# Optimization experiments

Measured on AMD Instinct MI355X. Metric: run time of the kernel, lower is better.

The kernel has to match this reference:

```python
import jax, jax.numpy as jnp
import numpy as np

N_NODES = 50000
N_EDGES = 800000
D = 101
L = 2
NEG_SLOPE = 0.2


def setup_inputs() -> dict:
    key = jax.random.key(0)
    k1, k2, k3, k4, k5 = jax.random.split(key, 5)
    x = jax.random.normal(k1, (N_NODES, D), dtype=jnp.float32)
    edge_index = jax.random.randint(k2, (2, N_EDGES), 0, N_NODES, dtype=jnp.int64)
    # Glorot-ish scaled params, one set per layer
    Ws = jax.random.normal(k3, (L, D, D), dtype=jnp.float32) / np.sqrt(D)
    att_src = jax.random.normal(k4, (L, D), dtype=jnp.float32) / np.sqrt(D)
    att_dst = jax.random.normal(k5, (L, D), dtype=jnp.float32) / np.sqrt(D)
    bias = jnp.zeros((L, D), dtype=jnp.float32)
    return {"x": x, "edge_index": edge_index, "Ws": Ws,
            "att_src": att_src, "att_dst": att_dst, "bias": bias}


def _gat_layer(x, W, a_src, a_dst, b, src, dst):
    # x: [N, D]; src/dst: [E'] (self-loops included)
    h = x @ W                                   # [N, D]
    alpha_s = h @ a_src                         # [N]
    alpha_d = h @ a_dst                         # [N]
    e = alpha_s[src] + alpha_d[dst]             # [E']
    e = jnp.where(e > 0, e, NEG_SLOPE * e)      # leaky_relu
    # segment softmax over edges grouped by destination node
    m = jax.ops.segment_max(e, dst, num_segments=N_NODES)   # [N]
    w = jnp.exp(e - m[dst])                                 # [E']
    z = jax.ops.segment_sum(w, dst, num_segments=N_NODES)   # [N]
    coef = w / (z[dst] + 1e-16)                             # [E']
    out = jax.ops.segment_sum(h[src] * coef[:, None], dst,
                              num_segments=N_NODES)         # [N, D]
    return out + b


def reference(x, edge_index, Ws, att_src, att_dst, bias):
    # Add self-loops once (PyG GATConv default add_self_loops=True)
    loops = jnp.arange(N_NODES, dtype=edge_index.dtype)
    src = jnp.concatenate([edge_index[0], loops])
    dst = jnp.concatenate([edge_index[1], loops])
    for l in range(L):
        x = _gat_layer(x, Ws[l], att_src[l], att_dst[l], bias[l], src, dst)
    return x
```

## Files before the change

kernel.cpp:

```cpp
#include <hip/hip_runtime.h>
#include <math.h>

#define NN 50000
#define NE 800000
#define ET (NE + NN)
#define DF 101
#define HP 104
#define NEG 0.2f
#define MAXK 8

#define GM 64
#define KP 128
#define NP 112
#define LSTR 136

typedef __attribute__((ext_vector_type(8))) short bf16x8;
typedef __attribute__((ext_vector_type(4))) float f32x4;

__device__ __forceinline__ unsigned short f2bf(float f) {
    unsigned u = __float_as_uint(f);
    unsigned r = u + 0x7FFFu + ((u >> 16) & 1u);
    return (unsigned short)(r >> 16);
}
__device__ __forceinline__ float bflo(unsigned v) { return __uint_as_float(v << 16); }
__device__ __forceinline__ float bfhi(unsigned v) { return __uint_as_float(v & 0xFFFF0000u); }

__global__ __launch_bounds__(256) void proj_a(
    const float* __restrict__ W, const float* __restrict__ a_s,
    const float* __restrict__ a_d,
    float* __restrict__ wa_s, float* __restrict__ wa_d)
{
    int k = blockIdx.x * 4 + (threadIdx.x >> 6);
    if (k >= DF) return;
    int lane = threadIdx.x & 63;
    const float* wr = W + (size_t)k * DF;
    float w0 = wr[lane];
    float w1 = (lane < DF - 64) ? wr[64 + lane] : 0.f;
    float s1 = (lane < DF - 64) ? a_s[64 + lane] : 0.f;
    float d1 = (lane < DF - 64) ? a_d[64 + lane] : 0.f;
    float ps = w0 * a_s[lane] + w1 * s1;
    float pd = w0 * a_d[lane] + w1 * d1;
    #pragma unroll
    for (int off = 32; off; off >>= 1) {
        ps += __shfl_xor(ps, off);
        pd += __shfl_xor(pd, off);
    }
    if (lane == 0) { wa_s[k] = ps; wa_d[k] = pd; }
}

__global__ __launch_bounds__(256) void alpha_n(
    const float* __restrict__ x, const float* __restrict__ wa_s,
    const float* __restrict__ wa_d,
    float* __restrict__ as_n, float* __restrict__ ad_n)
{
    int n = blockIdx.x * 4 + (threadIdx.x >> 6);
    if (n >= NN) return;
    int lane = threadIdx.x & 63;
    const float* xr = x + (size_t)n * DF;
    float x0 = xr[lane];
    float x1v = (lane < DF - 64) ? xr[64 + lane] : 0.f;
    float s1  = (lane < DF - 64) ? wa_s[64 + lane] : 0.f;
    float d1  = (lane < DF - 64) ? wa_d[64 + lane] : 0.f;
    float ps = x0 * wa_s[lane] + x1v * s1;
    float pd = x0 * wa_d[lane] + x1v * d1;
    #pragma unroll
    for (int off = 32; off; off >>= 1) {
        ps += __shfl_xor(ps, off);
        pd += __shfl_xor(pd, off);
    }
    if (lane == 0) { as_n[n] = ps; ad_n[n] = pd; }
}

__global__ void prep_wt(const float* __restrict__ W, unsigned short* __restrict__ wtb) {
    int i = blockIdx.x * 256 + threadIdx.x;
    if (i >= NP * KP) return;
    int c = i >> 7;
    int k = i & (KP - 1);
    float v = (c < DF && k < DF) ? W[k * DF + c] : 0.f;
    wtb[c * KP + k] = f2bf(v);
}

__global__ __launch_bounds__(256) void gemm_h(
    const float* __restrict__ x, const unsigned short* __restrict__ wtb,
    unsigned short* __restrict__ h16)
{
    __shared__ unsigned short xs[GM * LSTR];
    __shared__ unsigned short ws[NP * LSTR];
    const int t = threadIdx.x;
    const int row0 = blockIdx.x * GM;

    {
        const uint4* src = (const uint4*)wtb;
        for (int i = t; i < NP * 16; i += 256) {
            int r = i >> 4, seg = i & 15;
            uint4 v = src[r * 16 + seg];
            *(uint4*)&ws[r * LSTR + seg * 8] = v;
        }
    }
    for (int i = t; i < GM * KP; i += 256) {
        int r = i >> 7, k = i & (KP - 1);
        int row = row0 + r;
        float v = (k < DF && row < NN) ? x[(size_t)row * DF + k] : 0.f;
        xs[r * LSTR + k] = f2bf(v);
    }
    __syncthreads();

    const int wv = t >> 6, lane = t & 63;
    const int arow = wv * 16 + (lane & 15);
    const int kgrp = (lane >> 4) * 8;

    bf16x8 a[4];
    #pragma unroll
    for (int ks = 0; ks < 4; ++ks)
        a[ks] = *(const bf16x8*)&xs[arow * LSTR + ks * 32 + kgrp];

    #pragma unroll
    for (int nt = 0; nt < 7; ++nt) {
        f32x4 acc = {0.f, 0.f, 0.f, 0.f};
        const int col = nt * 16 + (lane & 15);
        #pragma unroll
        for (int ks = 0; ks < 4; ++ks) {
            bf16x8 b = *(const bf16x8*)&ws[col * LSTR + ks * 32 + kgrp];
            acc = __builtin_amdgcn_mfma_f32_16x16x32_bf16(a[ks], b, acc, 0, 0, 0);
        }
        const int rbase = row0 + wv * 16 + (lane >> 4) * 4;
        #pragma unroll
        for (int r = 0; r < 4; ++r) {
            int row = rbase + r;
            if (col < HP && row < NN)
                h16[(size_t)row * HP + col] = f2bf(acc[r]);
        }
    }
}


__global__ void count_rank(const int* __restrict__ ei, int* __restrict__ deg,
                           unsigned short* __restrict__ rank) {
    int i = blockIdx.x * blockDim.x + threadIdx.x;
    if (i >= ET) return;
    int d = (i < NE) ? ei[NE + i] : (i - NE);
    rank[i] = (unsigned short)atomicAdd(&deg[d], 1);
}

__global__ __launch_bounds__(256) void scanA(const int* __restrict__ deg,
                                             int* __restrict__ part, int* __restrict__ aux) {
    __shared__ int sh[256];
    int t = threadIdx.x;
    int i = blockIdx.x * 256 + t;
    int v = (i < NN) ? deg[i] : 0;
    sh[t] = v; __syncthreads();
    #pragma unroll
    for (int off = 1; off < 256; off <<= 1) {
        int u = (t >= off) ? sh[t - off] : 0;
        __syncthreads();
        sh[t] += u;
        __syncthreads();
    }
    if (i < NN) part[i] = sh[t];
    if (t == 255) aux[blockIdx.x] = sh[255];
}

__global__ __launch_bounds__(256) void scanB(const int* __restrict__ aux,
                                             int* __restrict__ auxex, int nb) {
    __shared__ int sh[256];
    int t = threadIdx.x;
    int v = (t < nb) ? aux[t] : 0;
    sh[t] = v; __syncthreads();
    #pragma unroll
    for (int off = 1; off < 256; off <<= 1) {
        int u = (t >= off) ? sh[t - off] : 0;
        __syncthreads();
        sh[t] += u;
        __syncthreads();
    }
    if (t < nb) auxex[t] = sh[t] - v;
}

__global__ void scanC(const int* __restrict__ part, const int* __restrict__ auxex,
                      int* __restrict__ rowptr) {
    int i = blockIdx.x * blockDim.x + threadIdx.x;
    if (i == 0) rowptr[0] = 0;
    if (i < NN) rowptr[i + 1] = part[i] + auxex[i >> 8];
}

__global__ void scatter_plain(const int* __restrict__ ei, const int* __restrict__ rowptr,
                              const unsigned short* __restrict__ rank,
                              int* __restrict__ srclist) {
    int i = blockIdx.x * blockDim.x + threadIdx.x;
    if (i >= ET) return;
    int s, d;
    if (i < NE) { s = ei[i]; d = ei[NE + i]; } else { s = d = i - NE; }
    srclist[rowptr[d] + rank[i]] = s;
}

__global__ __launch_bounds__(256) void gat_agg(
    const int* __restrict__ rowptr, const int* __restrict__ srclist,
    const float* __restrict__ a_s, const float* __restrict__ a_d,
    const unsigned short* __restrict__ h16, const float* __restrict__ bias,
    float* __restrict__ out)
{
    __shared__ __align__(16) uint2 ls[4][64];
    const int wv = threadIdx.x >> 6;
    int d = blockIdx.x * 4 + wv;
    if (d >= NN) return;
    int lane = threadIdx.x & 63;
    int s0 = rowptr[d], s1 = rowptr[d + 1];
    float ad = a_d[d];

    float earr[MAXK];
    int mysrc[MAXK];
    float mymax = -INFINITY;
    #pragma unroll
    for (int k = 0; k < MAXK; ++k) {
        int j = s0 + lane + k * 64;
        if (j < s1) {
            int s = srclist[j];
            mysrc[k] = s;
            float e = a_s[s] + ad;
            e = e > 0.f ? e : NEG * e;
            earr[k] = e;
            mymax = fmaxf(mymax, e);
        }
    }
    #pragma unroll
    for (int off = 32; off; off >>= 1)
        mymax = fmaxf(mymax, __shfl_xor(mymax, off));

    float sum = 0.f;
    #pragma unroll
    for (int k = 0; k < MAXK; ++k) {
        int j = s0 + lane + k * 64;
        if (j < s1) {
            float w = __expf(earr[k] - mymax);
            earr[k] = w;
            sum += w;
        }
    }
    #pragma unroll
    for (int off = 32; off; off >>= 1)
        sum += __shfl_xor(sum, off);
    float invz = 1.f / (sum + 1e-16f);

    const int li = (lane < 51) ? lane : 51;
    float acc0 = 0.f, acc1 = 0.f;
    #pragma unroll
    for (int k = 0; k < MAXK; ++k) {
        int jb = s0 + k * 64;
        if (jb >= s1) break;
        int lim = s1 - jb; if (lim > 64) lim = 64;
        ls[wv][lane] = make_uint2(__float_as_uint(earr[k] * invz),
                                  (unsigned)mysrc[k]);

        int i = 0;
        for (; i + 8 <= lim; i += 8) {
            uint4 q0 = *(const uint4*)&ls[wv][i];
            uint4 q1 = *(const uint4*)&ls[wv][i + 2];
            uint4 q2 = *(const uint4*)&ls[wv][i + 4];
            uint4 q3 = *(const uint4*)&ls[wv][i + 6];
            unsigned v0 = *((const unsigned*)(h16 + (size_t)q0.y * HP) + li);
            unsigned v1 = *((const unsigned*)(h16 + (size_t)q0.w * HP) + li);
            unsigned v2 = *((const unsigned*)(h16 + (size_t)q1.y * HP) + li);
            unsigned v3 = *((const unsigned*)(h16 + (size_t)q1.w * HP) + li);
            unsigned v4 = *((const unsigned*)(h16 + (size_t)q2.y * HP) + li);
            unsigned v5 = *((const unsigned*)(h16 + (size_t)q2.w * HP) + li);
            unsigned v6 = *((const unsigned*)(h16 + (size_t)q3.y * HP) + li);
            unsigned v7 = *((const unsigned*)(h16 + (size_t)q3.w * HP) + li);
            float c0 = __uint_as_float(q0.x), c1 = __uint_as_float(q0.z);
            float c2 = __uint_as_float(q1.x), c3 = __uint_as_float(q1.z);
            float c4 = __uint_as_float(q2.x), c5 = __uint_as_float(q2.z);
            float c6 = __uint_as_float(q3.x), c7 = __uint_as_float(q3.z);
            acc0 = fmaf(c0, bflo(v0), acc0); acc1 = fmaf(c0, bfhi(v0), acc1);
            acc0 = fmaf(c1, bflo(v1), acc0); acc1 = fmaf(c1, bfhi(v1), acc1);
            acc0 = fmaf(c2, bflo(v2), acc0); acc1 = fmaf(c2, bfhi(v2), acc1);
            acc0 = fmaf(c3, bflo(v3), acc0); acc1 = fmaf(c3, bfhi(v3), acc1);
            acc0 = fmaf(c4, bflo(v4), acc0); acc1 = fmaf(c4, bfhi(v4), acc1);
            acc0 = fmaf(c5, bflo(v5), acc0); acc1 = fmaf(c5, bfhi(v5), acc1);
            acc0 = fmaf(c6, bflo(v6), acc0); acc1 = fmaf(c6, bfhi(v6), acc1);
            acc0 = fmaf(c7, bflo(v7), acc0); acc1 = fmaf(c7, bfhi(v7), acc1);
        }
        for (; i + 4 <= lim; i += 4) {
            uint4 q0 = *(const uint4*)&ls[wv][i];
            uint4 q1 = *(const uint4*)&ls[wv][i + 2];
            unsigned v0 = *((const unsigned*)(h16 + (size_t)q0.y * HP) + li);
            unsigned v1 = *((const unsigned*)(h16 + (size_t)q0.w * HP) + li);
            unsigned v2 = *((const unsigned*)(h16 + (size_t)q1.y * HP) + li);
            unsigned v3 = *((const unsigned*)(h16 + (size_t)q1.w * HP) + li);
            float c0 = __uint_as_float(q0.x), c1 = __uint_as_float(q0.z);
            float c2 = __uint_as_float(q1.x), c3 = __uint_as_float(q1.z);
            acc0 = fmaf(c0, bflo(v0), acc0); acc1 = fmaf(c0, bfhi(v0), acc1);
            acc0 = fmaf(c1, bflo(v1), acc0); acc1 = fmaf(c1, bfhi(v1), acc1);
            acc0 = fmaf(c2, bflo(v2), acc0); acc1 = fmaf(c2, bfhi(v2), acc1);
            acc0 = fmaf(c3, bflo(v3), acc0); acc1 = fmaf(c3, bfhi(v3), acc1);
        }
        for (; i < lim; ++i) {
            uint2 p = ls[wv][i];
            unsigned v = *((const unsigned*)(h16 + (size_t)p.y * HP) + li);
            float c = __uint_as_float(p.x);
            acc0 = fmaf(c, bflo(v), acc0);
            acc1 = fmaf(c, bfhi(v), acc1);
        }
    }
    int c0 = 2 * lane;
    if (c0 < DF)     out[(size_t)d * DF + c0]     = acc0 + bias[c0];
    if (c0 + 1 < DF) out[(size_t)d * DF + c0 + 1] = acc1 + bias[c0 + 1];
}

static inline size_t alignup(size_t v) { return (v + 255) & ~size_t(255); }

extern "C" void kernel_launch(void* const* d_in, const int* in_sizes, int n_in,
                              void* d_out, int out_size, void* d_ws, size_t ws_size,
                              hipStream_t stream)
{
    const float* x    = (const float*)d_in[0];
    const int*   ei   = (const int*)  d_in[1];
    const float* Ws   = (const float*)d_in[2];
    const float* a_s  = (const float*)d_in[3];
    const float* a_d  = (const float*)d_in[4];
    const float* bias = (const float*)d_in[5];
    float* out = (float*)d_out;

    char* w = (char*)d_ws;
    unsigned short* h16  = (unsigned short*)w; w += alignup((size_t)NN * HP * 2);
    float* x1      = (float*)w; w += alignup((size_t)NN * DF * 4);
    int*   srclist = (int*)w;   w += alignup((size_t)ET * 4);
    unsigned short* rank = (unsigned short*)w; w += alignup((size_t)ET * 2);
    unsigned short* wtb0 = (unsigned short*)w; w += alignup((size_t)NP * KP * 2);
    unsigned short* wtb1 = (unsigned short*)w; w += alignup((size_t)NP * KP * 2);
    float* as_n    = (float*)w; w += alignup((size_t)NN * 4);
    float* ad_n    = (float*)w; w += alignup((size_t)NN * 4);
    int*   deg     = (int*)w;   w += alignup((size_t)NN * 4);
    int*   part    = (int*)w;   w += alignup((size_t)NN * 4);
    int*   rowptr  = (int*)w;   w += alignup((size_t)(NN + 1) * 4);
    int*   aux     = (int*)w;   w += alignup(256 * 4);
    int*   auxex   = (int*)w;   w += alignup(256 * 4);
    float* wa_s    = (float*)w; w += alignup(DF * 4);
    float* wa_d    = (float*)w; w += alignup(DF * 4);

    const int NB = (NN + 255) / 256;
    const int NWT = (NP * KP + 255) / 256;

    prep_wt<<<NWT, 256, 0, stream>>>(Ws,               wtb0);
    prep_wt<<<NWT, 256, 0, stream>>>(Ws + DF * DF,     wtb1);

    hipMemsetAsync(deg, 0, (size_t)NN * 4, stream);
    count_rank<<<(ET + 255) / 256, 256, 0, stream>>>(ei, deg, rank);
    scanA<<<NB, 256, 0, stream>>>(deg, part, aux);
    scanB<<<1, 256, 0, stream>>>(aux, auxex, NB);
    scanC<<<NB, 256, 0, stream>>>(part, auxex, rowptr);
    scatter_plain<<<(ET + 255) / 256, 256, 0, stream>>>(ei, rowptr, rank, srclist);

    for (int l = 0; l < 2; ++l) {
        const float* curx = (l == 0) ? x : x1;
        float*       nxt  = (l == 0) ? x1 : out;
        const float* Wl   = Ws + l * DF * DF;
        const unsigned short* wtb = (l == 0) ? wtb0 : wtb1;

        proj_a<<<(DF + 3) / 4, 256, 0, stream>>>(Wl, a_s + l * DF, a_d + l * DF,
                                                 wa_s, wa_d);
        alpha_n<<<(NN + 3) / 4, 256, 0, stream>>>(curx, wa_s, wa_d, as_n, ad_n);
        gemm_h<<<(NN + GM - 1) / GM, 256, 0, stream>>>(curx, wtb, h16);
        gat_agg<<<(NN + 3) / 4, 256, 0, stream>>>(rowptr, srclist, as_n, ad_n,
                                                  h16, bias + l * DF, nxt);
    }
}
```

Baseline: 302.6 us.

## Fuse attention logit computation into GEMM epilogue and deepen gather unroll

Removes the separate proj_a and alpha_n kernels. The per-node attention scores are now computed inside gemm_h from the MFMA accumulators, multiplied by a_src and a_dst held in shared memory and reduced across the 16-lane groups with shuffles. This saves two launches per layer and a full extra read of x. The cost is that the scores now come from the bf16-input GEMM result instead of fp32 x·(W·a), which is slightly less precise. The aggregation loop also gains a 16-edge unrolled path so more gathers are in flight at once, at the cost of more registers.

```diff
diff --git a/kernel.cpp b/kernel.cpp
--- a/kernel.cpp
+++ b/kernel.cpp
@@ -25,52 +25,6 @@
 __device__ __forceinline__ float bflo(unsigned v) { return __uint_as_float(v << 16); }
 __device__ __forceinline__ float bfhi(unsigned v) { return __uint_as_float(v & 0xFFFF0000u); }
 
-__global__ __launch_bounds__(256) void proj_a(
-    const float* __restrict__ W, const float* __restrict__ a_s,
-    const float* __restrict__ a_d,
-    float* __restrict__ wa_s, float* __restrict__ wa_d)
-{
-    int k = blockIdx.x * 4 + (threadIdx.x >> 6);
-    if (k >= DF) return;
-    int lane = threadIdx.x & 63;
-    const float* wr = W + (size_t)k * DF;
-    float w0 = wr[lane];
-    float w1 = (lane < DF - 64) ? wr[64 + lane] : 0.f;
-    float s1 = (lane < DF - 64) ? a_s[64 + lane] : 0.f;
-    float d1 = (lane < DF - 64) ? a_d[64 + lane] : 0.f;
-    float ps = w0 * a_s[lane] + w1 * s1;
-    float pd = w0 * a_d[lane] + w1 * d1;
-    #pragma unroll
-    for (int off = 32; off; off >>= 1) {
-        ps += __shfl_xor(ps, off);
-        pd += __shfl_xor(pd, off);
-    }
-    if (lane == 0) { wa_s[k] = ps; wa_d[k] = pd; }
-}
-
-__global__ __launch_bounds__(256) void alpha_n(
-    const float* __restrict__ x, const float* __restrict__ wa_s,
-    const float* __restrict__ wa_d,
-    float* __restrict__ as_n, float* __restrict__ ad_n)
-{
-    int n = blockIdx.x * 4 + (threadIdx.x >> 6);
-    if (n >= NN) return;
-    int lane = threadIdx.x & 63;
-    const float* xr = x + (size_t)n * DF;
-    float x0 = xr[lane];
-    float x1v = (lane < DF - 64) ? xr[64 + lane] : 0.f;
-    float s1  = (lane < DF - 64) ? wa_s[64 + lane] : 0.f;
-    float d1  = (lane < DF - 64) ? wa_d[64 + lane] : 0.f;
-    float ps = x0 * wa_s[lane] + x1v * s1;
-    float pd = x0 * wa_d[lane] + x1v * d1;
-    #pragma unroll
-    for (int off = 32; off; off >>= 1) {
-        ps += __shfl_xor(ps, off);
-        pd += __shfl_xor(pd, off);
-    }
-    if (lane == 0) { as_n[n] = ps; ad_n[n] = pd; }
-}
-
 __global__ void prep_wt(const float* __restrict__ W, unsigned short* __restrict__ wtb) {
     int i = blockIdx.x * 256 + threadIdx.x;
     if (i >= NP * KP) return;
@@ -82,13 +36,20 @@
 
 __global__ __launch_bounds__(256) void gemm_h(
     const float* __restrict__ x, const unsigned short* __restrict__ wtb,
-    unsigned short* __restrict__ h16)
+    const float* __restrict__ a_s, const float* __restrict__ a_d,
+    unsigned short* __restrict__ h16,
+    float* __restrict__ alpha_s, float* __restrict__ alpha_d)
 {
     __shared__ unsigned short xs[GM * LSTR];
     __shared__ unsigned short ws[NP * LSTR];
+    __shared__ float asv[NP], adv[NP];
     const int t = threadIdx.x;
     const int row0 = blockIdx.x * GM;
 
+    if (t < NP) {
+        asv[t] = (t < DF) ? a_s[t] : 0.f;
+        adv[t] = (t < DF) ? a_d[t] : 0.f;
+    }
     {
         const uint4* src = (const uint4*)wtb;
         for (int i = t; i < NP * 16; i += 256) {
@@ -113,6 +74,10 @@
     #pragma unroll
     for (int ks = 0; ks < 4; ++ks)
         a[ks] = *(const bf16x8*)&xs[arow * LSTR + ks * 32 + kgrp];
+
+    float pas[4] = {0.f, 0.f, 0.f, 0.f};
+    float pad_[4] = {0.f, 0.f, 0.f, 0.f};
+    const int rbase = row0 + wv * 16 + (lane >> 4) * 4;
 
     #pragma unroll
     for (int nt = 0; nt < 7; ++nt) {
@@ -123,12 +88,30 @@
             bf16x8 b = *(const bf16x8*)&ws[col * LSTR + ks * 32 + kgrp];
             acc = __builtin_amdgcn_mfma_f32_16x16x32_bf16(a[ks], b, acc, 0, 0, 0);
         }
-        const int rbase = row0 + wv * 16 + (lane >> 4) * 4;
+        const float av = asv[col], dv = adv[col];
         #pragma unroll
         for (int r = 0; r < 4; ++r) {
             int row = rbase + r;
             if (col < HP && row < NN)
                 h16[(size_t)row * HP + col] = f2bf(acc[r]);
+            pas[r]  = fmaf(acc[r], av, pas[r]);
+            pad_[r] = fmaf(acc[r], dv, pad_[r]);
+        }
+    }
+
+    #pragma unroll
+    for (int off = 1; off < 16; off <<= 1) {
+        #pragma unroll
+        for (int r = 0; r < 4; ++r) {
+            pas[r]  += __shfl_xor(pas[r],  off);
+            pad_[r] += __shfl_xor(pad_[r], off);
+        }
+    }
+    if ((lane & 15) == 0) {
+        #pragma unroll
+        for (int r = 0; r < 4; ++r) {
+            int row = rbase + r;
+            if (row < NN) { alpha_s[row] = pas[r]; alpha_d[row] = pad_[r]; }
         }
     }
 }
@@ -252,31 +235,37 @@
                                   (unsigned)mysrc[k]);
 
         int i = 0;
+        for (; i + 16 <= lim; i += 16) {
+            unsigned vv[16]; float cc[16];
+            #pragma unroll
+            for (int u = 0; u < 8; ++u) {
+                uint4 q = *(const uint4*)&ls[wv][i + 2 * u];
+                cc[2*u]   = __uint_as_float(q.x);
+                cc[2*u+1] = __uint_as_float(q.z);
+                vv[2*u]   = *((const unsigned*)(h16 + (size_t)q.y * HP) + li);
+                vv[2*u+1] = *((const unsigned*)(h16 + (size_t)q.w * HP) + li);
+            }
+            #pragma unroll
+            for (int u = 0; u < 16; ++u) {
+                acc0 = fmaf(cc[u], bflo(vv[u]), acc0);
+                acc1 = fmaf(cc[u], bfhi(vv[u]), acc1);
+            }
+        }
         for (; i + 8 <= lim; i += 8) {
-            uint4 q0 = *(const uint4*)&ls[wv][i];
-            uint4 q1 = *(const uint4*)&ls[wv][i + 2];
-            uint4 q2 = *(const uint4*)&ls[wv][i + 4];
-            uint4 q3 = *(const uint4*)&ls[wv][i + 6];
-            unsigned v0 = *((const unsigned*)(h16 + (size_t)q0.y * HP) + li);
-            unsigned v1 = *((const unsigned*)(h16 + (size_t)q0.w * HP) + li);
-            unsigned v2 = *((const unsigned*)(h16 + (size_t)q1.y * HP) + li);
-            unsigned v3 = *((const unsigned*)(h16 + (size_t)q1.w * HP) + li);
-            unsigned v4 = *((const unsigned*)(h16 + (size_t)q2.y * HP) + li);
-            unsigned v5 = *((const unsigned*)(h16 + (size_t)q2.w * HP) + li);
-            unsigned v6 = *((const unsigned*)(h16 + (size_t)q3.y * HP) + li);
-            unsigned v7 = *((const unsigned*)(h16 + (size_t)q3.w * HP) + li);
-            float c0 = __uint_as_float(q0.x), c1 = __uint_as_float(q0.z);
-            float c2 = __uint_as_float(q1.x), c3 = __uint_as_float(q1.z);
-            float c4 = __uint_as_float(q2.x), c5 = __uint_as_float(q2.z);
-            float c6 = __uint_as_float(q3.x), c7 = __uint_as_float(q3.z);
-            acc0 = fmaf(c0, bflo(v0), acc0); acc1 = fmaf(c0, bfhi(v0), acc1);
-            acc0 = fmaf(c1, bflo(v1), acc0); acc1 = fmaf(c1, bfhi(v1), acc1);
-            acc0 = fmaf(c2, bflo(v2), acc0); acc1 = fmaf(c2, bfhi(v2), acc1);
-            acc0 = fmaf(c3, bflo(v3), acc0); acc1 = fmaf(c3, bfhi(v3), acc1);
-            acc0 = fmaf(c4, bflo(v4), acc0); acc1 = fmaf(c4, bfhi(v4), acc1);
-            acc0 = fmaf(c5, bflo(v5), acc0); acc1 = fmaf(c5, bfhi(v5), acc1);
-            acc0 = fmaf(c6, bflo(v6), acc0); acc1 = fmaf(c6, bfhi(v6), acc1);
-            acc0 = fmaf(c7, bflo(v7), acc0); acc1 = fmaf(c7, bfhi(v7), acc1);
+            unsigned vv[8]; float cc[8];
+            #pragma unroll
+            for (int u = 0; u < 4; ++u) {
+                uint4 q = *(const uint4*)&ls[wv][i + 2 * u];
+                cc[2*u]   = __uint_as_float(q.x);
+                cc[2*u+1] = __uint_as_float(q.z);
+                vv[2*u]   = *((const unsigned*)(h16 + (size_t)q.y * HP) + li);
+                vv[2*u+1] = *((const unsigned*)(h16 + (size_t)q.w * HP) + li);
+            }
+            #pragma unroll
+            for (int u = 0; u < 8; ++u) {
+                acc0 = fmaf(cc[u], bflo(vv[u]), acc0);
+                acc1 = fmaf(cc[u], bfhi(vv[u]), acc1);
+            }
         }
         for (; i + 4 <= lim; i += 4) {
             uint4 q0 = *(const uint4*)&ls[wv][i];
@@ -333,8 +322,6 @@
     int*   rowptr  = (int*)w;   w += alignup((size_t)(NN + 1) * 4);
     int*   aux     = (int*)w;   w += alignup(256 * 4);
     int*   auxex   = (int*)w;   w += alignup(256 * 4);
-    float* wa_s    = (float*)w; w += alignup(DF * 4);
-    float* wa_d    = (float*)w; w += alignup(DF * 4);
 
     const int NB = (NN + 255) / 256;
     const int NWT = (NP * KP + 255) / 256;
@@ -352,13 +339,10 @@
     for (int l = 0; l < 2; ++l) {
         const float* curx = (l == 0) ? x : x1;
         float*       nxt  = (l == 0) ? x1 : out;
-        const float* Wl   = Ws + l * DF * DF;
         const unsigned short* wtb = (l == 0) ? wtb0 : wtb1;
 
-        proj_a<<<(DF + 3) / 4, 256, 0, stream>>>(Wl, a_s + l * DF, a_d + l * DF,
-                                                 wa_s, wa_d);
-        alpha_n<<<(NN + 3) / 4, 256, 0, stream>>>(curx, wa_s, wa_d, as_n, ad_n);
-        gemm_h<<<(NN + GM - 1) / GM, 256, 0, stream>>>(curx, wtb, h16);
+        gemm_h<<<(NN + GM - 1) / GM, 256, 0, stream>>>(
+            curx, wtb, a_s + l * DF, a_d + l * DF, h16, as_n, ad_n);
         gat_agg<<<(NN + 3) / 4, 256, 0, stream>>>(rowptr, srclist, as_n, ad_n,
                                                   h16, bias + l * DF, nxt);
     }
```

After: 315.0 us. 1.04x slower.
